# Optimization experiments

Measured on AMD Instinct MI355X. Metric: run time of the kernel, lower is better.

The kernel has to match this reference:

```python
import jax, jax.numpy as jnp
import numpy as np

B, N, T, D = 64, 76, 128, 128
AH, HEADS, DFF, FAH = 8, 4, 512, 128
DK = D // HEADS


def layer_norm(x, a, b, eps=1e-7):
    mean = x.mean(-1, keepdims=True)
    std = jnp.std(x, -1, ddof=1, keepdims=True)  # torch.std is unbiased
    return a * (x - mean) / (std + eps) + b


def setup_inputs() -> dict:
    key = jax.random.key(0)
    ks = jax.random.split(key, 32)
    w = lambda i, shape, s=0.05: (jax.random.normal(ks[i], shape, jnp.float32) * s)
    return {
        "H": jax.random.normal(ks[0], (B, N, T, D), jnp.float32),
        "mask": jax.random.randint(ks[1], (B, N, T), 0, 2).astype(jnp.float32),
        "feature_mask": jax.random.uniform(ks[2], (B, N), dtype=jnp.float32),
        # MissingAwareTemporalAttention params (shared across features)
        "Wt": w(3, (D, AH), 0.1), "Wx": w(4, (D, AH), 0.1),
        "rate": jnp.array([0.8], jnp.float32),
        "obs_bias": jnp.float32(0.5), "miss_bias": jnp.float32(0.0),
        # MultiHeadedAttention params (weights stored [in,out])
        "Wq": w(5, (D, D)), "bq": jnp.zeros(D, jnp.float32),
        "Wk": w(6, (D, D)), "bk": jnp.zeros(D, jnp.float32),
        "Wv": w(7, (D, D)), "bv": jnp.zeros(D, jnp.float32),
        "Wo": w(8, (D, D)), "bo": jnp.zeros(D, jnp.float32),
        # SublayerConnection LayerNorms
        "ln1_a": jnp.ones(D, jnp.float32), "ln1_b": jnp.zeros(D, jnp.float32),
        "ln2_a": jnp.ones(D, jnp.float32), "ln2_b": jnp.zeros(D, jnp.float32),
        # PositionwiseFeedForward
        "w1": w(9, (D, DFF)), "b1": jnp.zeros(DFF, jnp.float32),
        "w2": w(10, (DFF, D)), "b2": jnp.zeros(D, jnp.float32),
        # FinalAttentionQKV ('mul')
        "fWq": w(11, (D, FAH)), "fbq": jnp.zeros(FAH, jnp.float32),
        "fWk": w(12, (D, FAH)), "fbk": jnp.zeros(FAH, jnp.float32),
        "fWv": w(13, (D, FAH)), "fbv": jnp.zeros(FAH, jnp.float32),
        "mask_scale": jnp.float32(1.0),
    }


def concare_forward(H, mask, feature_mask, Wt, Wx, rate, obs_bias, miss_bias,
                    Wq, bq, Wk, bk, Wv, bv, Wo, bo, ln1_a, ln1_b, ln2_a, ln2_b,
                    w1, b1, w2, b2, fWq, fbq, fWk, fbk, fWv, fbv, mask_scale):
    # ---- MissingAwareTemporalAttention per feature (vectorized over N) ----
    q = jnp.einsum('bnd,da->bna', H[:, :, -1, :], Wt)           # [B,N,AH]
    k = jnp.einsum('bntd,da->bnta', H, Wx)                      # [B,N,T,AH]
    dot = jnp.einsum('bna,bnta->bnt', q, k)                     # [B,N,T]
    b_time = (jnp.arange(T - 1, -1, -1, dtype=jnp.float32) + 1.0)  # [T]
    sig = jax.nn.sigmoid(dot)
    denom = jax.nn.sigmoid(rate[0]) * (jnp.log(2.72 + (1.0 - sig)) * b_time)
    e = jax.nn.relu(sig / denom)
    e = e + jnp.where(mask > 0.5, obs_bias, miss_bias)
    a = jax.nn.softmax(e, axis=-1)                              # over T
    emb = jnp.einsum('bnt,bntd->bnd', a, H)                     # [B,N,D]

    # ---- SublayerConnection 1: pre-norm + MultiHeadedAttention + residual ----
    x0 = layer_norm(emb, ln1_a, ln1_b)
    qh = (x0 @ Wq + bq).reshape(B, N, HEADS, DK).transpose(0, 2, 1, 3)
    kh = (x0 @ Wk + bk).reshape(B, N, HEADS, DK).transpose(0, 2, 1, 3)
    vh = (x0 @ Wv + bv).reshape(B, N, HEADS, DK).transpose(0, 2, 1, 3)
    scores = jnp.einsum('bhqd,bhkd->bhqk', qh, kh) / np.sqrt(DK)
    p = jax.nn.softmax(scores, axis=-1)
    ctx = jnp.einsum('bhqk,bhkd->bhqd', p, vh).transpose(0, 2, 1, 3).reshape(B, N, D)
    mha = ctx @ Wo + bo                                          # [B,N,D]
    # DeCov regularizer over batch, per feature position
    feats = jnp.transpose(mha, (1, 2, 0))                        # [N,D,B]
    centered = feats - feats.mean(axis=2, keepdims=True)
    cov = jnp.einsum('ndb,neb->nde', centered, centered) / (B - 1)
    diag = jnp.einsum('ndd->nd', cov)
    decov = 0.5 * (jnp.sum(cov ** 2) - jnp.sum(diag ** 2))
    x = emb + mha

    # ---- SublayerConnection 2: pre-norm + FFN + residual ----
    x1 = layer_norm(x, ln2_a, ln2_b)
    ffn = jax.nn.relu(x1 @ w1 + b1) @ w2 + b2
    x = x + ffn                                                  # [B,N,D]

    # ---- FinalAttentionQKV ('mul') ----
    fq = x[:, -1, :] @ fWq + fbq                                 # [B,FAH]
    fk = x @ fWk + fbk                                           # [B,N,FAH]
    fv = x @ fWv + fbv                                           # [B,N,FAH]
    fe = jnp.einsum('bna,ba->bn', fk, fq)
    fe = fe + mask_scale * feature_mask
    alpha = jax.nn.softmax(fe, axis=1)                           # over N
    pooled = jnp.einsum('bn,bna->ba', alpha, fv)                 # [B,FAH]
    return pooled, decov


def reference(H, mask, feature_mask, Wt, Wx, rate, obs_bias, miss_bias,
              Wq, bq, Wk, bk, Wv, bv, Wo, bo, ln1_a, ln1_b, ln2_a, ln2_b,
              w1, b1, w2, b2, fWq, fbq, fWk, fbk, fWv, fbv, mask_scale):
    return concare_forward(H, mask, feature_mask, Wt, Wx, rate, obs_bias, miss_bias,
                           Wq, bq, Wk, bk, Wv, bv, Wo, bo, ln1_a, ln1_b, ln2_a, ln2_b,
                           w1, b1, w2, b2, fWq, fbq, fWk, fbk, fWv, fbv, mask_scale)
```

## Files before the change

### kernel.cpp

```cpp
#include <hip/hip_runtime.h>
#include <hip/hip_bf16.h>
#include <math.h>

#define BB 64
#define NN 76
#define TT 128
#define DD 128
#define AH 8
#define NHEADS 4
#define DFF 512
#define FAH 128
#define DK 32
#define BN (BB*NN)
#define ROWS 8
#define NBLK (BN/ROWS)

__global__ __launch_bounds__(256, 4) void k1_temporal(
    const float* __restrict__ H, const float* __restrict__ mask,
    const float* __restrict__ Wt, const float* __restrict__ Wx,
    const float* __restrict__ rate, const float* __restrict__ obs_bias,
    const float* __restrict__ miss_bias, float* __restrict__ emb)
{
    __shared__ __align__(16) float wts[DD*AH];
    __shared__ __align__(16) float wxs[DD*AH];
    __shared__ __align__(16) float row127[DD];
    __shared__ __align__(16) float wqs[DD];
    __shared__ __align__(16) float dots[TT];
    __shared__ __align__(16) float as_[TT];
    __shared__ __align__(16) float parts[8][DD];
    __shared__ float qpart[2][AH];
    __shared__ float red[4];

    const int bid = blockIdx.x;
    const int tid = threadIdx.x;
    const size_t base = (size_t)bid * (TT*DD);

    float4 h[16];
    const float4* Hg4 = (const float4*)(H + base);
    #pragma unroll
    for (int j = 0; j < 16; ++j) h[j] = Hg4[j*256 + tid];

    for (int i = tid; i < DD*AH; i += 256) { wts[i] = Wt[i]; wxs[i] = Wx[i]; }
    if (tid < DD) row127[tid] = H[base + (TT-1)*DD + tid];
    __syncthreads();

    if (tid < DD) {
        const float r = row127[tid];
        float p[AH];
        #pragma unroll
        for (int a = 0; a < AH; ++a) p[a] = r * wts[tid*AH + a];
        #pragma unroll
        for (int a = 0; a < AH; ++a) {
            float v = p[a];
            #pragma unroll
            for (int m = 1; m < 64; m <<= 1) v += __shfl_xor(v, m, 64);
            if ((tid & 63) == 0) qpart[tid >> 6][a] = v;
        }
    }
    __syncthreads();
    if (tid < DD) {
        float acc = 0.f;
        #pragma unroll
        for (int a = 0; a < AH; ++a)
            acc += (qpart[0][a] + qpart[1][a]) * wxs[tid*AH + a];
        wqs[tid] = acc;
    }
    __syncthreads();

    const int c = tid & 31, g = tid >> 5;
    const float4 wq4 = *(const float4*)&wqs[4*c];
    #pragma unroll
    for (int j = 0; j < 16; ++j) {
        float p = h[j].x*wq4.x + h[j].y*wq4.y + h[j].z*wq4.z + h[j].w*wq4.w;
        #pragma unroll
        for (int m = 1; m < 32; m <<= 1) p += __shfl_xor(p, m, 64);
        if (c == 0) dots[g + 8*j] = p;
    }
    __syncthreads();

    float ev = 0.f;
    if (tid < TT) {
        const float dot = dots[tid];
        const float sig = 1.f / (1.f + expf(-dot));
        const float sr  = 1.f / (1.f + expf(-rate[0]));
        const float bt  = (float)(TT - tid);
        const float denom = sr * (logf(2.72f + (1.f - sig)) * bt);
        float e = fmaxf(sig / denom, 0.f);
        e += (mask[(size_t)bid*TT + tid] > 0.5f) ? obs_bias[0] : miss_bias[0];
        ev = e;
    }
    const int lane = tid & 63, w = tid >> 6;
    float vmax = (tid < TT) ? ev : -1e30f;
    #pragma unroll
    for (int m = 1; m < 64; m <<= 1) vmax = fmaxf(vmax, __shfl_xor(vmax, m, 64));
    if (lane == 0) red[w] = vmax;
    __syncthreads();
    const float mx = fmaxf(fmaxf(red[0], red[1]), fmaxf(red[2], red[3]));
    const float ex = (tid < TT) ? expf(ev - mx) : 0.f;
    float vs = ex;
    #pragma unroll
    for (int m = 1; m < 64; m <<= 1) vs += __shfl_xor(vs, m, 64);
    __syncthreads();
    if (lane == 0) red[w] = vs;
    __syncthreads();
    const float ssum = red[0] + red[1] + red[2] + red[3];
    if (tid < TT) as_[tid] = ex / ssum;
    __syncthreads();

    float4 facc = make_float4(0.f, 0.f, 0.f, 0.f);
    #pragma unroll
    for (int j = 0; j < 16; ++j) {
        const float a = as_[g + 8*j];
        facc.x += a*h[j].x; facc.y += a*h[j].y;
        facc.z += a*h[j].z; facc.w += a*h[j].w;
    }
    *(float4*)&parts[g][4*c] = facc;
    __syncthreads();
    if (tid < DD) {
        float acc = 0.f;
        #pragma unroll
        for (int gg = 0; gg < 8; ++gg) acc += parts[gg][tid];
        emb[(size_t)bid*DD + tid] = acc;
    }
}

__global__ __launch_bounds__(256) void k2a_ln_qkv(
    const float* __restrict__ emb,
    const float* __restrict__ ln_a, const float* __restrict__ ln_b,
    const float* __restrict__ Wq, const float* __restrict__ bq,
    const float* __restrict__ Wk, const float* __restrict__ bk,
    const float* __restrict__ Wv, const float* __restrict__ bv,
    float* __restrict__ qb, float* __restrict__ kb, float* __restrict__ vb)
{
    __shared__ float xs[ROWS][DD];
    const int tid = threadIdx.x;
    const int r0 = blockIdx.x * ROWS;

    for (int i = tid; i < ROWS*DD; i += 256) {
        const int r = i / DD, d = i % DD;
        xs[r][d] = emb[(size_t)(r0+r)*DD + d];
    }
    __syncthreads();

    {
        const int wv_ = tid >> 6, lane = tid & 63;
        for (int rr = 0; rr < 2; ++rr) {
            const int r = wv_*2 + rr;
            const float x0 = xs[r][lane], x1 = xs[r][lane+64];
            float s = x0 + x1;
            #pragma unroll
            for (int m = 1; m < 64; m <<= 1) s += __shfl_xor(s, m, 64);
            const float mean = s / (float)DD;
            const float d0 = x0 - mean, d1 = x1 - mean;
            float v = d0*d0 + d1*d1;
            #pragma unroll
            for (int m = 1; m < 64; m <<= 1) v += __shfl_xor(v, m, 64);
            const float inv = 1.f / (sqrtf(v / (float)(DD-1)) + 1e-7f);
            xs[r][lane]    = ln_a[lane]   * (d0*inv) + ln_b[lane];
            xs[r][lane+64] = ln_a[lane+64]* (d1*inv) + ln_b[lane+64];
        }
    }
    __syncthreads();

    const int j = tid & 127, half = tid >> 7, rbase = half*4;
    float aq[4] = {0,0,0,0}, ak[4] = {0,0,0,0}, av[4] = {0,0,0,0};
    for (int d = 0; d < DD; ++d) {
        const float wqv = Wq[d*DD+j], wkv = Wk[d*DD+j], wvv = Wv[d*DD+j];
        #pragma unroll
        for (int r = 0; r < 4; ++r) {
            const float xv = xs[rbase+r][d];
            aq[r] += xv*wqv; ak[r] += xv*wkv; av[r] += xv*wvv;
        }
    }
    const float bqv = bq[j], bkv = bk[j], bvv = bv[j];
    #pragma unroll
    for (int r = 0; r < 4; ++r) {
        const size_t o = (size_t)(r0 + rbase + r)*DD + j;
        qb[o] = aq[r]+bqv; kb[o] = ak[r]+bkv; vb[o] = av[r]+bvv;
    }
}

__global__ __launch_bounds__(128) void k2b_attn(
    const float* __restrict__ qb, const float* __restrict__ kb,
    const float* __restrict__ vb, float* __restrict__ ctx)
{
    __shared__ float Qs[NN][DK], Ks[NN][DK], Vs[NN][DK];
    __shared__ float Ps[NN][NN+1];
    const int b = blockIdx.x / NHEADS, h = blockIdx.x % NHEADS;
    const int tid = threadIdx.x;
    const int co = h*DK;

    for (int i = tid; i < NN*DK; i += 128) {
        const int r = i / DK, c = i % DK;
        const size_t o = (size_t)(b*NN + r)*DD + co + c;
        Qs[r][c] = qb[o]; Ks[r][c] = kb[o]; Vs[r][c] = vb[o];
    }
    __syncthreads();

    const float scale = 0.17677669529663687f;
    if (tid < NN) {
        float qr[DK];
        #pragma unroll
        for (int c = 0; c < DK; ++c) qr[c] = Qs[tid][c];
        float mx = -1e30f;
        for (int k = 0; k < NN; ++k) {
            float s = 0.f;
            #pragma unroll
            for (int c = 0; c < DK; ++c) s += qr[c]*Ks[k][c];
            s *= scale;
            Ps[tid][k] = s;
            mx = fmaxf(mx, s);
        }
        float sum = 0.f;
        for (int k = 0; k < NN; ++k) { const float e = expf(Ps[tid][k]-mx); Ps[tid][k] = e; sum += e; }
        const float inv = 1.f/sum;
        float acc[DK];
        #pragma unroll
        for (int c = 0; c < DK; ++c) acc[c] = 0.f;
        for (int k = 0; k < NN; ++k) {
            const float p = Ps[tid][k];
            #pragma unroll
            for (int c = 0; c < DK; ++c) acc[c] += p*Vs[k][c];
        }
        const size_t o = (size_t)(b*NN + tid)*DD + co;
        #pragma unroll
        for (int c = 0; c < DK; ++c) ctx[o+c] = acc[c]*inv;
    }
}

__global__ __launch_bounds__(256) void k2c_proj_res(
    const float* __restrict__ ctx, const float* __restrict__ emb,
    const float* __restrict__ Wo, const float* __restrict__ bo,
    float* __restrict__ mha, float* __restrict__ x)
{
    __shared__ float cs[ROWS][DD];
    const int tid = threadIdx.x;
    const int r0 = blockIdx.x * ROWS;
    for (int i = tid; i < ROWS*DD; i += 256) {
        const int r = i / DD, d = i % DD;
        cs[r][d] = ctx[(size_t)(r0+r)*DD + d];
    }
    __syncthreads();
    const int j = tid & 127, half = tid >> 7, rbase = half*4;
    float acc[4] = {0,0,0,0};
    for (int d = 0; d < DD; ++d) {
        const float wv = Wo[d*DD+j];
        #pragma unroll
        for (int r = 0; r < 4; ++r) acc[r] += cs[rbase+r][d]*wv;
    }
    const float bov = bo[j];
    #pragma unroll
    for (int r = 0; r < 4; ++r) {
        const size_t o = (size_t)(r0+rbase+r)*DD + j;
        const float m = acc[r] + bov;
        mha[o] = m;
        x[o] = emb[o] + m;
    }
}

__global__ __launch_bounds__(256) void k_decov(
    const float* __restrict__ mha, float* __restrict__ partial)
{
    __shared__ float Cs[BB][DD];
    __shared__ float means[DD];
    __shared__ float reda[256];
    __shared__ float redb[256];
    const int n = blockIdx.x, dc = blockIdx.y;
    const int tid = threadIdx.x;
    for (int i = tid; i < BB*DD; i += 256) {
        const int bb = i / DD, d = i % DD;
        Cs[bb][d] = mha[((size_t)bb*NN + n)*DD + d];
    }
    __syncthreads();
    if (tid < DD) {
        float s = 0.f;
        for (int bb = 0; bb < BB; ++bb) s += Cs[bb][tid];
        means[tid] = s / (float)BB;
    }
    __syncthreads();
    if (tid < DD) {
        const float m = means[tid];
        for (int bb = 0; bb < BB; ++bb) Cs[bb][tid] -= m;
    }
    __syncthreads();
    float ss = 0.f, dd2 = 0.f;
    const float invB1 = 1.f/63.f;
    for (int qi = tid; qi < 1024; qi += 256) {
        const int d  = dc*32 + qi / 32;
        const int e4 = (qi % 32) * 4;
        float a0=0,a1=0,a2=0,a3=0;
        for (int bb = 0; bb < BB; ++bb) {
            const float cd = Cs[bb][d];
            const float4 ce = *(const float4*)&Cs[bb][e4];
            a0 += cd*ce.x; a1 += cd*ce.y; a2 += cd*ce.z; a3 += cd*ce.w;
        }
        a0*=invB1; a1*=invB1; a2*=invB1; a3*=invB1;
        ss += a0*a0+a1*a1+a2*a2+a3*a3;
        if (d >= e4 && d < e4+4) {
            const float c[4] = {a0,a1,a2,a3};
            const float cd = c[d-e4];
            dd2 += cd*cd;
        }
    }
    reda[tid] = ss; redb[tid] = dd2;
    __syncthreads();
    for (int s2 = 128; s2 >= 1; s2 >>= 1) {
        if (tid < s2) { reda[tid] += reda[tid+s2]; redb[tid] += redb[tid+s2]; }
        __syncthreads();
    }
    if (tid == 0) partial[n*4 + dc] = 0.5f*(reda[0] - redb[0]);
}

__global__ __launch_bounds__(256) void k3_ffn(
    const float* __restrict__ x,
    const float* __restrict__ ln_a, const float* __restrict__ ln_b,
    const float* __restrict__ w1, const float* __restrict__ b1,
    const float* __restrict__ w2, const float* __restrict__ b2,
    float* __restrict__ x2)
{
    __shared__ float xs[ROWS][DD];
    __shared__ float x1s[ROWS][DD];
    __shared__ float hs[ROWS][DFF];
    __shared__ float parts[2][ROWS][DD];
    const int tid = threadIdx.x;
    const int r0 = blockIdx.x * ROWS;
    for (int i = tid; i < ROWS*DD; i += 256) {
        const int r = i / DD, d = i % DD;
        xs[r][d] = x[(size_t)(r0+r)*DD + d];
    }
    __syncthreads();
    {
        const int wv_ = tid >> 6, lane = tid & 63;
        for (int rr = 0; rr < 2; ++rr) {
            const int r = wv_*2 + rr;
            const float v0 = xs[r][lane], v1 = xs[r][lane+64];
            float s = v0 + v1;
            #pragma unroll
            for (int m = 1; m < 64; m <<= 1) s += __shfl_xor(s, m, 64);
            const float mean = s / (float)DD;
            const float d0 = v0-mean, d1 = v1-mean;
            float vv = d0*d0 + d1*d1;
            #pragma unroll
            for (int m = 1; m < 64; m <<= 1) vv += __shfl_xor(vv, m, 64);
            const float inv = 1.f / (sqrtf(vv/(float)(DD-1)) + 1e-7f);
            x1s[r][lane]    = ln_a[lane]   * (d0*inv) + ln_b[lane];
            x1s[r][lane+64] = ln_a[lane+64]* (d1*inv) + ln_b[lane+64];
        }
    }
    __syncthreads();
    {
        float acc0[ROWS], acc1[ROWS];
        #pragma unroll
        for (int r = 0; r < ROWS; ++r) { acc0[r]=0.f; acc1[r]=0.f; }
        for (int d = 0; d < DD; ++d) {
            const float wv0 = w1[d*DFF + tid], wv1 = w1[d*DFF + tid + 256];
            #pragma unroll
            for (int r = 0; r < ROWS; ++r) {
                const float xv = x1s[r][d];
                acc0[r] += xv*wv0; acc1[r] += xv*wv1;
            }
        }
        const float b10 = b1[tid], b11 = b1[tid+256];
        #pragma unroll
        for (int r = 0; r < ROWS; ++r) {
            hs[r][tid]     = fmaxf(acc0[r]+b10, 0.f);
            hs[r][tid+256] = fmaxf(acc1[r]+b11, 0.f);
        }
    }
    __syncthreads();
    {
        const int j = tid & 127, half = tid >> 7;
        float acc[ROWS];
        #pragma unroll
        for (int r = 0; r < ROWS; ++r) acc[r] = 0.f;
        for (int k = half*256; k < half*256 + 256; ++k) {
            const float wv = w2[k*DD + j];
            #pragma unroll
            for (int r = 0; r < ROWS; ++r) acc[r] += hs[r][k]*wv;
        }
        #pragma unroll
        for (int r = 0; r < ROWS; ++r) parts[half][r][j] = acc[r];
        __syncthreads();
        if (half == 0) {
            const float b2v = b2[j];
            #pragma unroll
            for (int r = 0; r < ROWS; ++r) {
                const size_t o = (size_t)(r0+r)*DD + j;
                x2[o] = xs[r][j] + parts[0][r][j] + parts[1][r][j] + b2v;
            }
        }
    }
}

__global__ __launch_bounds__(128) void k4_final(
    const float* __restrict__ x, const float* __restrict__ feature_mask,
    const float* __restrict__ fWq, const float* __restrict__ fbq,
    const float* __restrict__ fWk, const float* __restrict__ fbk,
    const float* __restrict__ fWv, const float* __restrict__ fbv,
    const float* __restrict__ mask_scale, const float* __restrict__ decov_partial,
    float* __restrict__ out)
{
    __shared__ float Xs[NN][DD];
    __shared__ float fqs[DD], gs[DD], ys[DD];
    __shared__ float es[NN];
    __shared__ float sc[2];
    const int b = blockIdx.x;
    const int tid = threadIdx.x;
    for (int i = tid; i < NN*DD; i += 128) {
        const int r = i / DD, d = i % DD;
        Xs[r][d] = x[((size_t)b*NN + r)*DD + d];
    }
    __syncthreads();
    {
        float acc = 0.f;
        for (int d = 0; d < DD; ++d) acc += Xs[NN-1][d] * fWq[d*FAH + tid];
        fqs[tid] = acc + fbq[tid];
    }
    __syncthreads();
    {
        float acc = 0.f;
        for (int a = 0; a < FAH; ++a) acc += fWk[tid*FAH + a] * fqs[a];
        gs[tid] = acc;
    }
    if (tid == 0) {
        float acc = 0.f;
        for (int a = 0; a < FAH; ++a) acc += fbk[a]*fqs[a];
        sc[0] = acc;
    }
    __syncthreads();
    const float msc = mask_scale[0];
    if (tid < NN) {
        float acc = 0.f;
        for (int d = 0; d < DD; ++d) acc += Xs[tid][d]*gs[d];
        es[tid] = acc + sc[0] + msc * feature_mask[b*NN + tid];
    }
    __syncthreads();
    if (tid == 0) {
        float mx = -1e30f;
        for (int n2 = 0; n2 < NN; ++n2) mx = fmaxf(mx, es[n2]);
        float sum = 0.f;
        for (int n2 = 0; n2 < NN; ++n2) { const float e = expf(es[n2]-mx); es[n2] = e; sum += e; }
        sc[1] = 1.f/sum;
    }
    __syncthreads();
    {
        const float inv = sc[1];
        float acc = 0.f;
        for (int n2 = 0; n2 < NN; ++n2) acc += es[n2]*Xs[n2][tid];
        ys[tid] = acc * inv;
    }
    __syncthreads();
    {
        float acc = 0.f;
        for (int d = 0; d < DD; ++d) acc += ys[d]*fWv[d*FAH + tid];
        out[(size_t)b*FAH + tid] = acc + fbv[tid];
    }
    if (b == 0 && tid == 0) {
        float s = 0.f;
        for (int i = 0; i < NN*4; ++i) s += decov_partial[i];
        out[BB*FAH] = s;
    }
}

extern "C" void kernel_launch(void* const* d_in, const int* in_sizes, int n_in,
                              void* d_out, int out_size, void* d_ws, size_t ws_size,
                              hipStream_t stream) {
    const float* H    = (const float*)d_in[0];
    const float* mask = (const float*)d_in[1];
    const float* fm   = (const float*)d_in[2];
    const float* Wt   = (const float*)d_in[3];
    const float* Wx   = (const float*)d_in[4];
    const float* rate = (const float*)d_in[5];
    const float* obs_bias  = (const float*)d_in[6];
    const float* miss_bias = (const float*)d_in[7];
    const float* Wq = (const float*)d_in[8];   const float* bq = (const float*)d_in[9];
    const float* Wk = (const float*)d_in[10];  const float* bk = (const float*)d_in[11];
    const float* Wv = (const float*)d_in[12];  const float* bv = (const float*)d_in[13];
    const float* Wo = (const float*)d_in[14];  const float* bo = (const float*)d_in[15];
    const float* ln1a = (const float*)d_in[16]; const float* ln1b = (const float*)d_in[17];
    const float* ln2a = (const float*)d_in[18]; const float* ln2b = (const float*)d_in[19];
    const float* w1 = (const float*)d_in[20];  const float* b1 = (const float*)d_in[21];
    const float* w2 = (const float*)d_in[22];  const float* b2 = (const float*)d_in[23];
    const float* fWq = (const float*)d_in[24]; const float* fbq = (const float*)d_in[25];
    const float* fWk = (const float*)d_in[26]; const float* fbk = (const float*)d_in[27];
    const float* fWv = (const float*)d_in[28]; const float* fbv = (const float*)d_in[29];
    const float* mask_scale = (const float*)d_in[30];
    float* out = (float*)d_out;

    float* ws = (float*)d_ws;
    const size_t S = (size_t)BN*DD;
    float* emb = ws;
    float* qb  = ws + 1*S;
    float* kb  = ws + 2*S;
    float* vb  = ws + 3*S;
    float* ctx = ws + 4*S;
    float* mha = ws + 5*S;
    float* xb  = ws + 6*S;
    float* x2  = ws + 7*S;
    float* dpart = ws + 8*S;

    k1_temporal<<<BN, 256, 0, stream>>>(H, mask, Wt, Wx, rate, obs_bias, miss_bias, emb);
    k2a_ln_qkv<<<NBLK, 256, 0, stream>>>(emb, ln1a, ln1b, Wq, bq, Wk, bk, Wv, bv, qb, kb, vb);
    k2b_attn<<<BB*NHEADS, 128, 0, stream>>>(qb, kb, vb, ctx);
    k2c_proj_res<<<NBLK, 256, 0, stream>>>(ctx, emb, Wo, bo, mha, xb);
    k_decov<<<dim3(NN, 4), 256, 0, stream>>>(mha, dpart);
    k3_ffn<<<NBLK, 256, 0, stream>>>(xb, ln2a, ln2b, w1, b1, w2, b2, x2);
    k4_final<<<BB, 128, 0, stream>>>(x2, fm, fWq, fbq, fWk, fbk, fWv, fbv, mask_scale, dpart, out);
}
```

Measured before the change: 198.5 us.

## Widen temporal kernel to 512 threads and drop shared weight staging

```diff
diff --git a/kernel.cpp b/kernel.cpp
--- a/kernel.cpp
+++ b/kernel.cpp
@@ -15,40 +15,44 @@
 #define ROWS 8
 #define NBLK (BN/ROWS)
 
-__global__ __launch_bounds__(256, 4) void k1_temporal(
+__global__ __launch_bounds__(512, 6) void k1_temporal(
     const float* __restrict__ H, const float* __restrict__ mask,
     const float* __restrict__ Wt, const float* __restrict__ Wx,
     const float* __restrict__ rate, const float* __restrict__ obs_bias,
     const float* __restrict__ miss_bias, float* __restrict__ emb)
 {
-    __shared__ __align__(16) float wts[DD*AH];
-    __shared__ __align__(16) float wxs[DD*AH];
-    __shared__ __align__(16) float row127[DD];
     __shared__ __align__(16) float wqs[DD];
     __shared__ __align__(16) float dots[TT];
     __shared__ __align__(16) float as_[TT];
-    __shared__ __align__(16) float parts[8][DD];
+    __shared__ __align__(16) float parts[16][DD];
     __shared__ float qpart[2][AH];
-    __shared__ float red[4];
+    __shared__ float redmax[2];
+    __shared__ float redsum[2];
 
     const int bid = blockIdx.x;
     const int tid = threadIdx.x;
     const size_t base = (size_t)bid * (TT*DD);
 
-    float4 h[16];
+    float r127 = 0.f, maskv = 0.f;
+    float4 wt0, wt1, wx0, wx1;
+    if (tid < DD) {
+        r127 = H[base + (TT-1)*DD + tid];
+        wt0 = *(const float4*)&Wt[tid*AH + 0];
+        wt1 = *(const float4*)&Wt[tid*AH + 4];
+        wx0 = *(const float4*)&Wx[tid*AH + 0];
+        wx1 = *(const float4*)&Wx[tid*AH + 4];
+        maskv = mask[(size_t)bid*TT + tid];
+    }
+    const float ratev = rate[0], obsv = obs_bias[0], missv = miss_bias[0];
+
+    float4 h[8];
     const float4* Hg4 = (const float4*)(H + base);
     #pragma unroll
-    for (int j = 0; j < 16; ++j) h[j] = Hg4[j*256 + tid];
-
-    for (int i = tid; i < DD*AH; i += 256) { wts[i] = Wt[i]; wxs[i] = Wx[i]; }
-    if (tid < DD) row127[tid] = H[base + (TT-1)*DD + tid];
-    __syncthreads();
+    for (int j = 0; j < 8; ++j) h[j] = Hg4[j*512 + tid];
 
     if (tid < DD) {
-        const float r = row127[tid];
-        float p[AH];
-        #pragma unroll
-        for (int a = 0; a < AH; ++a) p[a] = r * wts[tid*AH + a];
+        float p[AH] = {r127*wt0.x, r127*wt0.y, r127*wt0.z, r127*wt0.w,
+                       r127*wt1.x, r127*wt1.y, r127*wt1.z, r127*wt1.w};
         #pragma unroll
         for (int a = 0; a < AH; ++a) {
             float v = p[a];
@@ -59,58 +63,60 @@
     }
     __syncthreads();
     if (tid < DD) {
-        float acc = 0.f;
-        #pragma unroll
-        for (int a = 0; a < AH; ++a)
-            acc += (qpart[0][a] + qpart[1][a]) * wxs[tid*AH + a];
-        wqs[tid] = acc;
+        const float q0 = qpart[0][0]+qpart[1][0], q1 = qpart[0][1]+qpart[1][1];
+        const float q2 = qpart[0][2]+qpart[1][2], q3 = qpart[0][3]+qpart[1][3];
+        const float q4 = qpart[0][4]+qpart[1][4], q5 = qpart[0][5]+qpart[1][5];
+        const float q6 = qpart[0][6]+qpart[1][6], q7 = qpart[0][7]+qpart[1][7];
+        wqs[tid] = q0*wx0.x + q1*wx0.y + q2*wx0.z + q3*wx0.w
+                 + q4*wx1.x + q5*wx1.y + q6*wx1.z + q7*wx1.w;
     }
     __syncthreads();
 
     const int c = tid & 31, g = tid >> 5;
     const float4 wq4 = *(const float4*)&wqs[4*c];
     #pragma unroll
-    for (int j = 0; j < 16; ++j) {
+    for (int j = 0; j < 8; ++j) {
         float p = h[j].x*wq4.x + h[j].y*wq4.y + h[j].z*wq4.z + h[j].w*wq4.w;
         #pragma unroll
         for (int m = 1; m < 32; m <<= 1) p += __shfl_xor(p, m, 64);
-        if (c == 0) dots[g + 8*j] = p;
-    }
-    __syncthreads();
-
-    float ev = 0.f;
+        if (c == 0) dots[g + 16*j] = p;
+    }
+    __syncthreads();
+
+    const int lane = tid & 63, w = tid >> 6;
+    float ev = -1e30f;
     if (tid < TT) {
         const float dot = dots[tid];
         const float sig = 1.f / (1.f + expf(-dot));
-        const float sr  = 1.f / (1.f + expf(-rate[0]));
+        const float sr  = 1.f / (1.f + expf(-ratev));
         const float bt  = (float)(TT - tid);
         const float denom = sr * (logf(2.72f + (1.f - sig)) * bt);
         float e = fmaxf(sig / denom, 0.f);
-        e += (mask[(size_t)bid*TT + tid] > 0.5f) ? obs_bias[0] : miss_bias[0];
+        e += (maskv > 0.5f) ? obsv : missv;
         ev = e;
-    }
-    const int lane = tid & 63, w = tid >> 6;
-    float vmax = (tid < TT) ? ev : -1e30f;
-    #pragma unroll
-    for (int m = 1; m < 64; m <<= 1) vmax = fmaxf(vmax, __shfl_xor(vmax, m, 64));
-    if (lane == 0) red[w] = vmax;
-    __syncthreads();
-    const float mx = fmaxf(fmaxf(red[0], red[1]), fmaxf(red[2], red[3]));
+        float vmax = ev;
+        #pragma unroll
+        for (int m = 1; m < 64; m <<= 1) vmax = fmaxf(vmax, __shfl_xor(vmax, m, 64));
+        if (lane == 0) redmax[w] = vmax;
+    }
+    __syncthreads();
+    const float mx = fmaxf(redmax[0], redmax[1]);
     const float ex = (tid < TT) ? expf(ev - mx) : 0.f;
-    float vs = ex;
-    #pragma unroll
-    for (int m = 1; m < 64; m <<= 1) vs += __shfl_xor(vs, m, 64);
-    __syncthreads();
-    if (lane == 0) red[w] = vs;
-    __syncthreads();
-    const float ssum = red[0] + red[1] + red[2] + red[3];
+    if (tid < TT) {
+        float vs = ex;
+        #pragma unroll
+        for (int m = 1; m < 64; m <<= 1) vs += __shfl_xor(vs, m, 64);
+        if (lane == 0) redsum[w] = vs;
+    }
+    __syncthreads();
+    const float ssum = redsum[0] + redsum[1];
     if (tid < TT) as_[tid] = ex / ssum;
     __syncthreads();
 
     float4 facc = make_float4(0.f, 0.f, 0.f, 0.f);
     #pragma unroll
-    for (int j = 0; j < 16; ++j) {
-        const float a = as_[g + 8*j];
+    for (int j = 0; j < 8; ++j) {
+        const float a = as_[g + 16*j];
         facc.x += a*h[j].x; facc.y += a*h[j].y;
         facc.z += a*h[j].z; facc.w += a*h[j].w;
     }
@@ -119,7 +125,7 @@
     if (tid < DD) {
         float acc = 0.f;
         #pragma unroll
-        for (int gg = 0; gg < 8; ++gg) acc += parts[gg][tid];
+        for (int gg = 0; gg < 16; ++gg) acc += parts[gg][tid];
         emb[(size_t)bid*DD + tid] = acc;
     }
 }
@@ -499,7 +505,7 @@
     float* x2  = ws + 7*S;
     float* dpart = ws + 8*S;
 
-    k1_temporal<<<BN, 256, 0, stream>>>(H, mask, Wt, Wx, rate, obs_bias, miss_bias, emb);
+    k1_temporal<<<BN, 512, 0, stream>>>(H, mask, Wt, Wx, rate, obs_bias, miss_bias, emb);
     k2a_ln_qkv<<<NBLK, 256, 0, stream>>>(emb, ln1a, ln1b, Wq, bq, Wk, bk, Wv, bv, qb, kb, vb);
     k2b_attn<<<BB*NHEADS, 128, 0, stream>>>(qb, kb, vb, ctx);
     k2c_proj_res<<<NBLK, 256, 0, stream>>>(ctx, emb, Wo, bo, mha, xb);
```

Measured after the change: 184.6 us. 7.0% less time.
